# Performance work log

Measured on AMD Instinct MI355X. Metric: run time of the kernel, lower is better.

Reference implementation:

```python
import jax, jax.numpy as jnp
import numpy as np


def setup_inputs() -> dict:
    key = jax.random.key(0)
    k1, k2, k3 = jax.random.split(key, 3)
    preds = jax.random.normal(k1, (8, 3, 2048, 8), dtype=jnp.float32)
    gts = jax.random.normal(k2, (8, 3, 2048), dtype=jnp.float32)
    idx = jax.random.randint(k3, (64, 2), 0, 8, dtype=jnp.int64)
    return {"preds": preds, "gts": gts, "idx": idx}


def reference(preds, gts, idx):
    # preds: [bs, 3, N, seeds], gts: [bs, 3, N], idx: [num, 2] (batch, seed)
    num = idx.shape[0]
    # select (batch, seed) pairs -> [num, 3, N]
    p = jnp.transpose(preds, (0, 3, 1, 2))[idx[:, 0], idx[:, 1]]
    # gts expanded over seeds is constant in seed -> just index batch
    g = gts[idx[:, 0]]  # [num, 3, N]
    x = jnp.transpose(p, (0, 2, 1))  # [num, N, 3]
    y = jnp.transpose(g, (0, 2, 1))  # [num, N, 3]
    # P[b, i, j] = ||x_i||^2 + ||y_j||^2 - 2 x_i . y_j
    rx = jnp.sum(x * x, axis=-1)  # [num, N]
    ry = jnp.sum(y * y, axis=-1)  # [num, N]
    zz = jnp.einsum('bid,bjd->bij', x, y)  # [num, N, N]
    P = rx[:, :, None] + ry[:, None, :] - 2.0 * zz
    loss_1 = jnp.sum(jnp.min(P, axis=1))  # min over x for each y
    loss_2 = jnp.sum(jnp.min(P, axis=2))  # min over y for each x
    return (loss_1 + loss_2) / num
```

## Files before the change

### kernel.cpp

```cpp
#include <hip/hip_runtime.h>


#define NPTS 2048
#define NB 64
#define BLK 256
#define NMIN (2 * NB * NPTS)

#define PREDS_A 49152
#define PREDS_C 16384
#define GTS_A 6144
#define GTS_C 2048

#define OFF_PARTIAL (NMIN * 4)
#define OFF_QPK     (OFF_PARTIAL + 4096)
#define OFF_YPK     (OFF_QPK + NB * NPTS * 32)
#define WS_REQ      (OFF_YPK + NB * NPTS * 32)

using bf16x8  = __attribute__((ext_vector_type(8))) __bf16;
using short8v = __attribute__((ext_vector_type(8))) short;
using f32x16  = __attribute__((ext_vector_type(16))) float;

static __device__ __forceinline__ unsigned short f2bf(float f) {
    unsigned u = __float_as_uint(f);
    u = u + 0x7FFFu + ((u >> 16) & 1u);
    return (unsigned short)(u >> 16);
}
static __device__ __forceinline__ float bf2f(unsigned short h) {
    return __uint_as_float(((unsigned)h) << 16);
}
static __device__ __forceinline__ float min3f(float a, float b, float c) {
    return fminf(fminf(a, b), c);
}
static __device__ __forceinline__ float ctree(f32x16 a) {
    const float c0 = min3f(a[0], a[1], a[2]);
    const float c1 = min3f(a[3], a[4], a[5]);
    const float c2 = min3f(a[6], a[7], a[8]);
    const float c3 = min3f(a[9], a[10], a[11]);
    const float c4 = min3f(a[12], a[13], a[14]);
    const float d0 = min3f(c0, c1, a[15]);
    const float d1 = min3f(c2, c3, c4);
    return fminf(d0, d1);
}

__global__ __launch_bounds__(256) void cf_pack(
    const float* __restrict__ preds, const float* __restrict__ gts,
    const int* __restrict__ idx, unsigned* __restrict__ colbuf,
    unsigned short* __restrict__ qpk, unsigned short* __restrict__ ypk)
{
    const int blk = blockIdx.x, tid = threadIdx.x;
    const unsigned short one = 0x3F80;
    if (blk < 512) {
        colbuf[blk * 256 + tid] = 0x7F800000u;
    } else if (blk < 1024) {
        const int p = (blk - 512) * 256 + tid;
        const int b = p >> 11, i = p & 2047;
        const int i0 = idx[2 * b], m1 = idx[2 * b + 1];
        const float* pb = preds + i0 * PREDS_A + m1 + i * 8;
        const float x0 = pb[0], x1 = pb[PREDS_C], x2 = pb[2 * PREDS_C];
        const float rx = fmaf(x0, x0, fmaf(x1, x1, x2 * x2));
        const float a0 = -2.f * x0, a1 = -2.f * x1, a2 = -2.f * x2;
        const unsigned short h0 = f2bf(a0), h1 = f2bf(a1), h2 = f2bf(a2);
        const unsigned short l0 = f2bf(a0 - bf2f(h0));
        const unsigned short l1 = f2bf(a1 - bf2f(h1));
        const unsigned short l2 = f2bf(a2 - bf2f(h2));
        const unsigned short rh = f2bf(rx), rl = f2bf(rx - bf2f(rh));
        alignas(16) unsigned short t[16] =
            {h0, h1, h2, h0, h1, h2, l0, l1, l2, rh, rl, one, one, 0, 0, 0};
        uint4* dst = (uint4*)(qpk + (size_t)p * 16);
        dst[0] = *(const uint4*)&t[0];
        dst[1] = *(const uint4*)&t[8];
    } else {
        const int p = (blk - 1024) * 256 + tid;
        const int b = p >> 11, j = p & 2047;
        const int i0 = idx[2 * b];
        const float* gb = gts + i0 * GTS_A + j;
        const float y0 = gb[0], y1 = gb[GTS_C], y2 = gb[2 * GTS_C];
        const float ry = fmaf(y0, y0, fmaf(y1, y1, y2 * y2));
        const unsigned short h0 = f2bf(y0), h1 = f2bf(y1), h2 = f2bf(y2);
        const unsigned short l0 = f2bf(y0 - bf2f(h0));
        const unsigned short l1 = f2bf(y1 - bf2f(h1));
        const unsigned short l2 = f2bf(y2 - bf2f(h2));
        const unsigned short rh = f2bf(ry), rl = f2bf(ry - bf2f(rh));
        alignas(16) unsigned short t[16] =
            {h0, h1, h2, l0, l1, l2, h0, h1, h2, one, one, rh, rl, 0, 0, 0};
        uint4* dst = (uint4*)(ypk + (size_t)p * 16);
        dst[0] = *(const uint4*)&t[0];
        dst[1] = *(const uint4*)&t[8];
    }
}

__global__ __launch_bounds__(BLK, 4) void cf_mf3(
    const unsigned short* __restrict__ qpk, const unsigned short* __restrict__ ypk,
    unsigned* __restrict__ minbuf)
{
    const int tid = threadIdx.x;
    const int bid = blockIdx.x;
    const int strip = bid & 15;
    const int b = bid >> 4;

    __shared__ unsigned scolw[NPTS];
    for (int k = tid; k < NPTS; k += BLK) scolw[k] = 0x7F800000u;

    const int l = tid & 63, w = tid >> 6;
    const int lc = l & 31, lh = l >> 5;

    const short8v* qv = (const short8v*)qpk;
    const short8v* yv = (const short8v*)ypk;

    const int arow = b * NPTS + strip * 128 + w * 32 + lc;
    const bf16x8 afrag = __builtin_bit_cast(bf16x8, qv[arow * 2 + lh]);

    float rm[16];
#pragma unroll
    for (int r = 0; r < 16; ++r) rm[r] = INFINITY;

    const f32x16 z = {0.f, 0.f, 0.f, 0.f, 0.f, 0.f, 0.f, 0.f,
                      0.f, 0.f, 0.f, 0.f, 0.f, 0.f, 0.f, 0.f};

    __syncthreads();

    const int ybase = b * NPTS * 2 + lc * 2 + lh;
#pragma unroll 2
    for (int s = 0; s < 32; ++s) {
        const bf16x8 bfA = __builtin_bit_cast(bf16x8, yv[ybase + (2 * s) * 64]);
        const bf16x8 bfB = __builtin_bit_cast(bf16x8, yv[ybase + (2 * s + 1) * 64]);
        f32x16 accA = __builtin_amdgcn_mfma_f32_32x32x16_bf16(afrag, bfA, z, 0, 0, 0);
        f32x16 accB = __builtin_amdgcn_mfma_f32_32x32x16_bf16(afrag, bfB, z, 0, 0, 0);
#pragma unroll
        for (int r = 0; r < 16; ++r) rm[r] = min3f(accA[r], accB[r], rm[r]);
        const float cmA = ctree(accA);
        const float cmB = ctree(accB);
        atomicMin(&scolw[(2 * s) * 32 + lc], __float_as_uint(fmaxf(cmA, 0.f)));
        atomicMin(&scolw[(2 * s + 1) * 32 + lc], __float_as_uint(fmaxf(cmB, 0.f)));
    }

    unsigned* rowbuf = minbuf;
    unsigned* colbuf = minbuf + NB * NPTS;

#pragma unroll
    for (int r = 0; r < 16; ++r) {
        float v = rm[r];
        v = fminf(v, __shfl_xor(v, 1, 32));
        v = fminf(v, __shfl_xor(v, 2, 32));
        v = fminf(v, __shfl_xor(v, 4, 32));
        v = fminf(v, __shfl_xor(v, 8, 32));
        v = fminf(v, __shfl_xor(v, 16, 32));
        rm[r] = v;
    }
    if (lc == 0) {
        const int rbase = b * NPTS + strip * 128 + w * 32 + 4 * lh;
#pragma unroll
        for (int r = 0; r < 16; ++r)
            rowbuf[rbase + (r & 3) + 8 * (r >> 2)] = __float_as_uint(fmaxf(rm[r], 0.f));
    }

    __syncthreads();
    for (int k = tid; k < NPTS; k += BLK)
        atomicMin(&colbuf[b * NPTS + k], scolw[k]);
}

#define FIT 128
#define FJT 128
#define PADI(j) ((j) + ((j) >> 4))

__global__ __launch_bounds__(256) void cf_init(unsigned* __restrict__ colbuf) {
    int i = blockIdx.x * 256 + threadIdx.x;
    colbuf[i] = 0x7F800000u;
}

__global__ __launch_bounds__(BLK, 4) void cf_tile_lds(
    const float* __restrict__ preds, const float* __restrict__ gts,
    const int* __restrict__ idx, unsigned* __restrict__ minbuf)
{
    const int tid = threadIdx.x;
    const int bid = blockIdx.x;
    const int it = bid & 15;
    const int b = bid >> 4;
    const int i0 = idx[2 * b];
    const int m1 = idx[2 * b + 1];
    const float* pbase = preds + i0 * PREDS_A + m1;
    const float* gbase = gts + i0 * GTS_A;

    __shared__ float4 sq[PADI(FIT - 1) + 2];
    __shared__ float4 sr[PADI(NPTS - 1) + 2];
    __shared__ float  scolw[4][FJT];

    if (tid < FIT) {
        const int i = it * FIT + tid;
        const float q0 = pbase[i * 8];
        const float q1 = pbase[i * 8 + PREDS_C];
        const float q2 = pbase[i * 8 + 2 * PREDS_C];
        const float rq = fmaf(q0, q0, fmaf(q1, q1, q2 * q2));
        sq[PADI(tid)] = make_float4(-2.f * q0, -2.f * q1, -2.f * q2, rq);
    }
#pragma unroll
    for (int k = 0; k < 8; ++k) {
        const int j = tid + BLK * k;
        const float r0 = gbase[j];
        const float r1 = gbase[j + GTS_C];
        const float r2 = gbase[j + 2 * GTS_C];
        const float rr = fmaf(r0, r0, fmaf(r1, r1, r2 * r2));
        sr[PADI(j)] = make_float4(r0, r1, r2, rr);
    }
    __syncthreads();

    const int ty = tid >> 4, tx = tid & 15;
    float nq0[8], nq1[8], nq2[8], rq[8], rmin[8];
#pragma unroll
    for (int u = 0; u < 8; ++u) {
        const float4 q = sq[PADI(ty * 8 + u)];
        nq0[u] = q.x; nq1[u] = q.y; nq2[u] = q.z; rq[u] = q.w;
        rmin[u] = INFINITY;
    }
    unsigned* rowbuf = minbuf;
    unsigned* colbuf = minbuf + NB * NPTS;

    for (int jt = 0; jt < NPTS / FJT; ++jt) {
        float4 r[8];
        const int rb = PADI(jt * FJT + tx * 8);
#pragma unroll
        for (int v = 0; v < 8; ++v) r[v] = sr[rb + v];
        float cmin[8];
#pragma unroll
        for (int v = 0; v < 8; ++v) cmin[v] = INFINITY;
#pragma unroll
        for (int v = 0; v < 8; v += 2) {
#pragma unroll
            for (int u = 0; u < 8; u += 2) {
                float s00 = fmaf(nq2[u], r[v].z, r[v].w);
                s00 = fmaf(nq1[u], r[v].y, s00);
                s00 = fmaf(nq0[u], r[v].x, s00);
                float s01 = fmaf(nq2[u], r[v + 1].z, r[v + 1].w);
                s01 = fmaf(nq1[u], r[v + 1].y, s01);
                s01 = fmaf(nq0[u], r[v + 1].x, s01);
                float s10 = fmaf(nq2[u + 1], r[v].z, r[v].w);
                s10 = fmaf(nq1[u + 1], r[v].y, s10);
                s10 = fmaf(nq0[u + 1], r[v].x, s10);
                float s11 = fmaf(nq2[u + 1], r[v + 1].z, r[v + 1].w);
                s11 = fmaf(nq1[u + 1], r[v + 1].y, s11);
                s11 = fmaf(nq0[u + 1], r[v + 1].x, s11);
                rmin[u]     = min3f(s00, s01, rmin[u]);
                rmin[u + 1] = min3f(s10, s11, rmin[u + 1]);
                const float d00 = s00 + rq[u];
                const float d10 = s10 + rq[u + 1];
                const float d01 = s01 + rq[u];
                const float d11 = s11 + rq[u + 1];
                cmin[v]     = min3f(d00, d10, cmin[v]);
                cmin[v + 1] = min3f(d01, d11, cmin[v + 1]);
            }
        }
#pragma unroll
        for (int v = 0; v < 8; ++v) {
            float c = cmin[v];
            c = fminf(c, __shfl_xor(c, 16, 64));
            c = fminf(c, __shfl_xor(c, 32, 64));
            cmin[v] = c;
        }
        if (((tid >> 4) & 3) == 0) {
            const int w = tid >> 6;
            *(float4*)&scolw[w][tx * 8]     = make_float4(cmin[0], cmin[1], cmin[2], cmin[3]);
            *(float4*)&scolw[w][tx * 8 + 4] = make_float4(cmin[4], cmin[5], cmin[6], cmin[7]);
        }
        __syncthreads();
        if (tid < FJT) {
            float m = fminf(min3f(scolw[0][tid], scolw[1][tid], scolw[2][tid]), scolw[3][tid]);
            m = fmaxf(m, 0.0f);
            atomicMin(&colbuf[b * NPTS + jt * FJT + tid], __float_as_uint(m));
        }
        __syncthreads();
    }
#pragma unroll
    for (int u = 0; u < 8; ++u) {
        float rm = rmin[u];
        rm = fminf(rm, __shfl_xor(rm, 1, 16));
        rm = fminf(rm, __shfl_xor(rm, 2, 16));
        rm = fminf(rm, __shfl_xor(rm, 4, 16));
        rm = fminf(rm, __shfl_xor(rm, 8, 16));
        rmin[u] = rm;
    }
    if (tx == 0) {
#pragma unroll
        for (int u = 0; u < 8; ++u) {
            const float d = fmaxf(rmin[u] + rq[u], 0.0f);
            rowbuf[b * NPTS + it * FIT + ty * 8 + u] = __float_as_uint(d);
        }
    }
}

__global__ __launch_bounds__(256) void cf_reduce1(const unsigned* __restrict__ minbuf,
                                                  float* __restrict__ partial) {
    __shared__ float sm[4];
    const int base = blockIdx.x * 1024;
    float s = 0.0f;
    for (int k = threadIdx.x; k < 1024; k += 256)
        s += __uint_as_float(minbuf[base + k]);
#pragma unroll
    for (int off = 32; off > 0; off >>= 1)
        s += __shfl_down(s, off, 64);
    if ((threadIdx.x & 63) == 0) sm[threadIdx.x >> 6] = s;
    __syncthreads();
    if (threadIdx.x == 0)
        partial[blockIdx.x] = sm[0] + sm[1] + sm[2] + sm[3];
}

__global__ __launch_bounds__(256) void cf_reduce2(const float* __restrict__ partial,
                                                  float* __restrict__ out) {
    __shared__ float sm[4];
    float s = partial[threadIdx.x];
#pragma unroll
    for (int off = 32; off > 0; off >>= 1)
        s += __shfl_down(s, off, 64);
    if ((threadIdx.x & 63) == 0) sm[threadIdx.x >> 6] = s;
    __syncthreads();
    if (threadIdx.x == 0)
        out[0] = (sm[0] + sm[1] + sm[2] + sm[3]) * (1.0f / 64.0f);
}

extern "C" void kernel_launch(void* const* d_in, const int* in_sizes, int n_in,
                              void* d_out, int out_size, void* d_ws, size_t ws_size,
                              hipStream_t stream) {
    const float* preds = (const float*)d_in[0];
    const float* gts   = (const float*)d_in[1];
    const int*   idx   = (const int*)d_in[2];
    float* out = (float*)d_out;

    unsigned* minbuf = (unsigned*)d_ws;
    unsigned* colbuf = minbuf + NB * NPTS;
    float* partial   = (float*)((char*)d_ws + OFF_PARTIAL);

    if (ws_size >= (size_t)WS_REQ) {
        unsigned short* qpk = (unsigned short*)((char*)d_ws + OFF_QPK);
        unsigned short* ypk = (unsigned short*)((char*)d_ws + OFF_YPK);
        cf_pack<<<1536, 256, 0, stream>>>(preds, gts, idx, colbuf, qpk, ypk);
        cf_mf3<<<NB * 16, BLK, 0, stream>>>(qpk, ypk, minbuf);
    } else {
        cf_init<<<(NB * NPTS) / 256, 256, 0, stream>>>(colbuf);
        cf_tile_lds<<<NB * (NPTS / FIT), BLK, 0, stream>>>(preds, gts, idx, minbuf);
    }
    cf_reduce1<<<NMIN / 1024, 256, 0, stream>>>(minbuf, partial);
    cf_reduce2<<<1, 256, 0, stream>>>(partial, out);
}
```

Baseline: 39.27 us.

## Replace column-min atomics with per-wave LDS slots and per-strip partial buffers

Column minima are no longer combined with shared-memory atomicMin and then global atomicMin. Each wave writes its column minima into its own LDS row after a cross-half shuffle, and each block writes a per-strip partial column array to global memory. The reduction kernel then takes the min across the 16 strips before summing. This removes atomic contention and the colbuf init pass, at the cost of a larger workspace (16x column partials) and more global traffic in the reduction.

```diff
diff --git a/kernel.cpp b/kernel.cpp
--- a/kernel.cpp
+++ b/kernel.cpp
@@ -4,17 +4,18 @@
 #define NPTS 2048
 #define NB 64
 #define BLK 256
-#define NMIN (2 * NB * NPTS)
 
 #define PREDS_A 49152
 #define PREDS_C 16384
 #define GTS_A 6144
 #define GTS_C 2048
 
-#define OFF_PARTIAL (NMIN * 4)
-#define OFF_QPK     (OFF_PARTIAL + 4096)
-#define OFF_YPK     (OFF_QPK + NB * NPTS * 32)
-#define WS_REQ      (OFF_YPK + NB * NPTS * 32)
+#define OFF_ROW   0
+#define OFF_CPART 524288
+#define OFF_PART  8912896
+#define OFF_QPK   8916992
+#define OFF_YPK   13111296
+#define WS_REQ    17305600
 
 using bf16x8  = __attribute__((ext_vector_type(8))) __bf16;
 using short8v = __attribute__((ext_vector_type(8))) short;
@@ -42,17 +43,15 @@
     return fminf(d0, d1);
 }
 
-__global__ __launch_bounds__(256) void cf_pack(
+__global__ __launch_bounds__(256) void cf_pack2(
     const float* __restrict__ preds, const float* __restrict__ gts,
-    const int* __restrict__ idx, unsigned* __restrict__ colbuf,
+    const int* __restrict__ idx,
     unsigned short* __restrict__ qpk, unsigned short* __restrict__ ypk)
 {
     const int blk = blockIdx.x, tid = threadIdx.x;
     const unsigned short one = 0x3F80;
     if (blk < 512) {
-        colbuf[blk * 256 + tid] = 0x7F800000u;
-    } else if (blk < 1024) {
-        const int p = (blk - 512) * 256 + tid;
+        const int p = blk * 256 + tid;
         const int b = p >> 11, i = p & 2047;
         const int i0 = idx[2 * b], m1 = idx[2 * b + 1];
         const float* pb = preds + i0 * PREDS_A + m1 + i * 8;
@@ -70,7 +69,7 @@
         dst[0] = *(const uint4*)&t[0];
         dst[1] = *(const uint4*)&t[8];
     } else {
-        const int p = (blk - 1024) * 256 + tid;
+        const int p = (blk - 512) * 256 + tid;
         const int b = p >> 11, j = p & 2047;
         const int i0 = idx[2 * b];
         const float* gb = gts + i0 * GTS_A + j;
@@ -89,17 +88,16 @@
     }
 }
 
-__global__ __launch_bounds__(BLK, 4) void cf_mf3(
+__global__ __launch_bounds__(BLK, 4) void cf_mf3b(
     const unsigned short* __restrict__ qpk, const unsigned short* __restrict__ ypk,
-    unsigned* __restrict__ minbuf)
+    float* __restrict__ rowbuf, float* __restrict__ colpart)
 {
     const int tid = threadIdx.x;
     const int bid = blockIdx.x;
     const int strip = bid & 15;
     const int b = bid >> 4;
 
-    __shared__ unsigned scolw[NPTS];
-    for (int k = tid; k < NPTS; k += BLK) scolw[k] = 0x7F800000u;
+    __shared__ float scolw[4][NPTS];
 
     const int l = tid & 63, w = tid >> 6;
     const int lc = l & 31, lh = l >> 5;
@@ -116,8 +114,6 @@
 
     const f32x16 z = {0.f, 0.f, 0.f, 0.f, 0.f, 0.f, 0.f, 0.f,
                       0.f, 0.f, 0.f, 0.f, 0.f, 0.f, 0.f, 0.f};
-
-    __syncthreads();
 
     const int ybase = b * NPTS * 2 + lc * 2 + lh;
 #pragma unroll 2
@@ -128,14 +124,13 @@
         f32x16 accB = __builtin_amdgcn_mfma_f32_32x32x16_bf16(afrag, bfB, z, 0, 0, 0);
 #pragma unroll
         for (int r = 0; r < 16; ++r) rm[r] = min3f(accA[r], accB[r], rm[r]);
-        const float cmA = ctree(accA);
-        const float cmB = ctree(accB);
-        atomicMin(&scolw[(2 * s) * 32 + lc], __float_as_uint(fmaxf(cmA, 0.f)));
-        atomicMin(&scolw[(2 * s + 1) * 32 + lc], __float_as_uint(fmaxf(cmB, 0.f)));
-    }
-
-    unsigned* rowbuf = minbuf;
-    unsigned* colbuf = minbuf + NB * NPTS;
+        float cmA = ctree(accA);
+        float cmB = ctree(accB);
+        cmA = fminf(cmA, __shfl_xor(cmA, 32, 64));
+        cmB = fminf(cmB, __shfl_xor(cmB, 32, 64));
+        scolw[w][(2 * s) * 32 + lc] = cmA;
+        scolw[w][(2 * s + 1) * 32 + lc] = cmB;
+    }
 
 #pragma unroll
     for (int r = 0; r < 16; ++r) {
@@ -151,14 +146,63 @@
         const int rbase = b * NPTS + strip * 128 + w * 32 + 4 * lh;
 #pragma unroll
         for (int r = 0; r < 16; ++r)
-            rowbuf[rbase + (r & 3) + 8 * (r >> 2)] = __float_as_uint(fmaxf(rm[r], 0.f));
-    }
-
-    __syncthreads();
-    for (int k = tid; k < NPTS; k += BLK)
-        atomicMin(&colbuf[b * NPTS + k], scolw[k]);
-}
-
+            rowbuf[rbase + (r & 3) + 8 * (r >> 2)] = fmaxf(rm[r], 0.f);
+    }
+
+    __syncthreads();
+    float* cp = colpart + (size_t)strip * (NB * NPTS) + b * NPTS;
+    for (int k = tid; k < NPTS; k += BLK) {
+        const float m = fminf(fminf(scolw[0][k], scolw[1][k]),
+                              fminf(scolw[2][k], scolw[3][k]));
+        cp[k] = fmaxf(m, 0.f);
+    }
+}
+
+__global__ __launch_bounds__(256) void cf_reduce1n(
+    const float* __restrict__ rowbuf, const float* __restrict__ colpart,
+    float* __restrict__ partial)
+{
+    __shared__ float sm[4];
+    const int blk = blockIdx.x, tid = threadIdx.x;
+    float s = 0.0f;
+    if (blk < 128) {
+        const int base = blk * 1024;
+        for (int i = 0; i < 4; ++i)
+            s += rowbuf[base + tid + i * 256];
+    } else {
+        const int base = (blk - 128) * 1024;
+        for (int i = 0; i < 4; ++i) {
+            const int g = base + tid + i * 256;
+            float m = INFINITY;
+#pragma unroll
+            for (int st = 0; st < 16; ++st)
+                m = fminf(m, colpart[(size_t)st * (NB * NPTS) + g]);
+            s += m;
+        }
+    }
+#pragma unroll
+    for (int off = 32; off > 0; off >>= 1)
+        s += __shfl_down(s, off, 64);
+    if ((tid & 63) == 0) sm[tid >> 6] = s;
+    __syncthreads();
+    if (tid == 0)
+        partial[blk] = sm[0] + sm[1] + sm[2] + sm[3];
+}
+
+__global__ __launch_bounds__(256) void cf_reduce2n(const float* __restrict__ partial,
+                                                   float* __restrict__ out) {
+    __shared__ float sm[4];
+    float s = partial[threadIdx.x];
+#pragma unroll
+    for (int off = 32; off > 0; off >>= 1)
+        s += __shfl_down(s, off, 64);
+    if ((threadIdx.x & 63) == 0) sm[threadIdx.x >> 6] = s;
+    __syncthreads();
+    if (threadIdx.x == 0)
+        out[0] = (sm[0] + sm[1] + sm[2] + sm[3]) * (1.0f / 64.0f);
+}
+
+#define NMIN (2 * NB * NPTS)
 #define FIT 128
 #define FJT 128
 #define PADI(j) ((j) + ((j) >> 4))
@@ -306,7 +350,7 @@
 __global__ __launch_bounds__(256) void cf_reduce2(const float* __restrict__ partial,
                                                   float* __restrict__ out) {
     __shared__ float sm[4];
-    float s = partial[threadIdx.x];
+    float s = (threadIdx.x < 128) ? partial[threadIdx.x] : 0.f;
 #pragma unroll
     for (int off = 32; off > 0; off >>= 1)
         s += __shfl_down(s, off, 64);
@@ -324,19 +368,23 @@
     const int*   idx   = (const int*)d_in[2];
     float* out = (float*)d_out;
 
-    unsigned* minbuf = (unsigned*)d_ws;
-    unsigned* colbuf = minbuf + NB * NPTS;
-    float* partial   = (float*)((char*)d_ws + OFF_PARTIAL);
-
     if (ws_size >= (size_t)WS_REQ) {
+        float* rowbuf  = (float*)((char*)d_ws + OFF_ROW);
+        float* colpart = (float*)((char*)d_ws + OFF_CPART);
+        float* partial = (float*)((char*)d_ws + OFF_PART);
         unsigned short* qpk = (unsigned short*)((char*)d_ws + OFF_QPK);
         unsigned short* ypk = (unsigned short*)((char*)d_ws + OFF_YPK);
-        cf_pack<<<1536, 256, 0, stream>>>(preds, gts, idx, colbuf, qpk, ypk);
-        cf_mf3<<<NB * 16, BLK, 0, stream>>>(qpk, ypk, minbuf);
+        cf_pack2<<<1024, 256, 0, stream>>>(preds, gts, idx, qpk, ypk);
+        cf_mf3b<<<NB * 16, BLK, 0, stream>>>(qpk, ypk, rowbuf, colpart);
+        cf_reduce1n<<<256, 256, 0, stream>>>(rowbuf, colpart, partial);
+        cf_reduce2n<<<1, 256, 0, stream>>>(partial, out);
     } else {
+        unsigned* minbuf = (unsigned*)d_ws;
+        unsigned* colbuf = minbuf + NB * NPTS;
+        float* partial   = (float*)((char*)d_ws + NMIN * 4);
         cf_init<<<(NB * NPTS) / 256, 256, 0, stream>>>(colbuf);
         cf_tile_lds<<<NB * (NPTS / FIT), BLK, 0, stream>>>(preds, gts, idx, minbuf);
-    }
-    cf_reduce1<<<NMIN / 1024, 256, 0, stream>>>(minbuf, partial);
-    cf_reduce2<<<1, 256, 0, stream>>>(partial, out);
-}
+        cf_reduce1<<<NMIN / 1024, 256, 0, stream>>>(minbuf, partial);
+        cf_reduce2<<<1, 256, 0, stream>>>(partial, out);
+    }
+}
```

Result: slower. 40.31 us (+2.6%).
